# Kernel tuning notes

Hardware: AMD Instinct MI355X
Metric: run time of the kernel (lower is better)

## Reference

```python
import jax, jax.numpy as jnp
import numpy as np

N, F, D, K = 4096, 128, 64, 2  # nodes, in_dim, out_dim, hops


def setup_inputs() -> dict:
    key = jax.random.key(0)
    k_x, k_a, k_e, k_w = jax.random.split(key, 4)
    X = jax.random.normal(k_x, (N, F), jnp.float32)
    # K+1 non-negative dense adjacency/distance matrices (stacked list)
    A = jax.random.uniform(k_a, (K + 1, N, N), jnp.float32)
    # Dense(out_dim, use_bias=False) weights, glorot-like scale
    W_emb = jax.random.normal(k_e, (F, D), jnp.float32) / np.sqrt(F)
    W_hops = jax.random.normal(k_w, (K + 1, F, D), jnp.float32) / np.sqrt(F)
    alpha = jnp.float32(0.1)
    return {"X": X, "A": A, "W_emb": W_emb, "W_hops": W_hops, "alpha": alpha}


def reference(X, A, W_emb, W_hops, alpha):
    # learned embeddings E = Dense(X)  -> [N, D]
    E = X @ W_emb
    # shared low-rank update alpha * E @ E^T  -> [N, N]
    low_rank = alpha * (E @ E.T)
    # per-hop kernel projections Dense_k(X)  -> [K+1, N, D]
    XW = jnp.einsum('nf,kfd->knd', X, W_hops)
    out = jnp.zeros((N, D), X.dtype)
    for k in range(A.shape[0]):  # fixed small K+1 hops
        A_hat = A[k] + low_rank                       # [N, N]
        deg = jnp.sum(A_hat, axis=1)                  # row sums
        d = jnp.power(deg, -0.5)                      # D^{-1/2}
        # D^{-1/2} A_hat D^{-1/2} via broadcast scaling (same math as diag matmuls)
        A_norm = d[:, None] * A_hat * d[None, :]
        out = out + A_norm @ XW[k]
    return jax.nn.relu(out)
```

## Files before the change

kernel.cpp:

```cpp
#include <hip/hip_runtime.h>
#include <math.h>

#define N_ 4096
#define F_ 128
#define D_ 64
#define KH_ 3
#define ZS_ 16
#define KC_ (N_ / ZS_)
#define BM_ 256

#define OFF_E      0
#define OFF_XW     (N_*D_)
#define OFF_SE     (OFF_XW + KH_*N_*D_)
#define OFF_T      (OFF_SE + D_)
#define OFF_RS     (OFF_T + KH_*D_*D_)
#define OFF_DVEC   (OFF_RS + KH_*N_)
#define OFF_YT     (OFF_DVEC + KH_*N_)
#define OFF_AYP    (OFF_YT + KH_*D_*N_/2)
#define OFF_ABF    (OFF_AYP + ZS_*KH_*N_*D_)

typedef __attribute__((ext_vector_type(8))) short bf16x8;
typedef __attribute__((ext_vector_type(4))) float f32x4;

static __device__ __forceinline__ unsigned short f2bf(float f) {
  union { float f; unsigned u; } v; v.f = f;
  unsigned r = (v.u + 0x7fffu + ((v.u >> 16) & 1u)) >> 16;
  return (unsigned short)r;
}

static __device__ __forceinline__ void gload_lds16(const unsigned short* g,
                                                   unsigned short* l) {
  __builtin_amdgcn_global_load_lds(
      (__attribute__((address_space(1))) unsigned int*)g,
      (__attribute__((address_space(3))) unsigned int*)l, 16, 0, 0);
}

__global__ __launch_bounds__(256) void degconv_kernel(
    const float* __restrict__ A, float* __restrict__ ws)
{
  if (blockIdx.x == 0) {
    for (int i = threadIdx.x; i < D_ + KH_ * D_ * D_; i += 256)
      ws[OFF_SE + i] = 0.f;
  }
  int lane = threadIdx.x & 63;
  int wave = threadIdx.x >> 6;
  int row = blockIdx.x * 4 + wave;
  const f32x4* Ar = (const f32x4*)(A + (size_t)row * N_);
  unsigned short* Br = (unsigned short*)(ws + OFF_ABF) + (size_t)row * N_;
  float s = 0.f;
#pragma unroll
  for (int it = 0; it < 8; ++it) {
    f32x4 v0 = __builtin_nontemporal_load(Ar + it * 128 + lane * 2 + 0);
    f32x4 v1 = __builtin_nontemporal_load(Ar + it * 128 + lane * 2 + 1);
    s += (v0[0] + v0[1]) + (v0[2] + v0[3]) + (v1[0] + v1[1]) + (v1[2] + v1[3]);
    union { unsigned short u[8]; uint4 q; } pk;
    pk.u[0] = f2bf(v0[0]); pk.u[1] = f2bf(v0[1]);
    pk.u[2] = f2bf(v0[2]); pk.u[3] = f2bf(v0[3]);
    pk.u[4] = f2bf(v1[0]); pk.u[5] = f2bf(v1[1]);
    pk.u[6] = f2bf(v1[2]); pk.u[7] = f2bf(v1[3]);
    *(uint4*)(Br + (size_t)it * 512 + lane * 8) = pk.q;
  }
#pragma unroll
  for (int off = 32; off > 0; off >>= 1)
    s += __shfl_xor(s, off);
  if (lane == 0) ws[OFF_RS + row] = s;
}

__global__ __launch_bounds__(256) void proj_kernel(
    const float* __restrict__ X, const float* __restrict__ W_emb,
    const float* __restrict__ W_hops, float* __restrict__ ws)
{
  __shared__ __align__(16) float sXT[32][68];
  __shared__ __align__(16) float sW[32][68];
  const int t = threadIdx.x;
  const int m = blockIdx.y;
  const int row0 = blockIdx.x * 64;
  const float* W = (m == 0) ? W_emb : (W_hops + (size_t)(m - 1) * F_ * D_);
  float* out = (m == 0) ? (ws + OFF_E) : (ws + OFF_XW + (size_t)(m - 1) * N_ * D_);
  const int tx = t & 15, ty = t >> 4;
  const int d0 = tx * 4, i0 = ty * 4;
  float acc[4][4] = {};
  for (int fc = 0; fc < F_; fc += 32) {
    {
      int i_l = t >> 3;
      int f_l = (t & 7) * 4;
      for (int r = 0; r < 2; ++r) {
        int i = i_l + r * 32;
        float4 v = *(const float4*)(X + (size_t)(row0 + i) * F_ + fc + f_l);
        sXT[f_l + 0][i] = v.x; sXT[f_l + 1][i] = v.y;
        sXT[f_l + 2][i] = v.z; sXT[f_l + 3][i] = v.w;
      }
      int f2 = t >> 4;
      int d  = (t & 15) * 4;
      for (int r = 0; r < 2; ++r) {
        int f = f2 + r * 16;
        *(float4*)&sW[f][d] = *(const float4*)(W + (size_t)(fc + f) * D_ + d);
      }
    }
    __syncthreads();
#pragma unroll 8
    for (int f = 0; f < 32; ++f) {
      float a[4], b[4];
      *(float4*)a = *(const float4*)&sXT[f][i0];
      *(float4*)b = *(const float4*)&sW[f][d0];
      for (int x = 0; x < 4; ++x)
        for (int y = 0; y < 4; ++y)
          acc[x][y] += a[x] * b[y];
    }
    __syncthreads();
  }
  for (int x = 0; x < 4; ++x)
    *(float4*)(out + (size_t)(row0 + i0 + x) * D_ + d0) = *(float4*)acc[x];
  if (m == 0) {
    float p[4];
    for (int y = 0; y < 4; ++y)
      p[y] = acc[0][y] + acc[1][y] + acc[2][y] + acc[3][y];
    *(float4*)&sXT[ty][d0] = *(float4*)p;
    __syncthreads();
    if (ty < 4) {
      int c = ty * 16 + tx;
      float s = 0.f;
#pragma unroll
      for (int r = 0; r < 16; ++r) s += sXT[r][c];
      atomicAdd(ws + OFF_SE + c, s);
    }
  }
}

__global__ __launch_bounds__(256) void prep_kernel(float* __restrict__ ws,
                                                   const float* __restrict__ alpha_p)
{
  const int k = blockIdx.y;
  const float* XWk = ws + OFF_XW + (size_t)k * N_ * D_;
  const float* E   = ws + OFF_E;
  const float* Sv  = ws + OFF_SE;
  const float* rs  = ws + OFF_RS + (size_t)k * N_;
  const float alpha = *alpha_p;
  int t = threadIdx.x;

  if (blockIdx.x < 64) {
    const int j0 = blockIdx.x * 64;
    unsigned short* Ytk = (unsigned short*)(ws + OFF_YT) + (size_t)k * D_ * N_;
    __shared__ float sS[64];
    __shared__ float d_l[64];
    __shared__ __align__(16) float sEy[64][65];
    __shared__ float sT[64][65];
    if (t < 64) sS[t] = Sv[t];
    {
      int j = t >> 2;
      int c0 = (t & 3) * 16;
      for (int r = 0; r < 4; ++r)
        *(float4*)&sEy[j][c0 + 4 * r] = *(const float4*)(E + (size_t)(j0 + j) * D_ + c0 + 4 * r);
    }
    __syncthreads();
    if (t < 64) {
      float dot = 0.f;
#pragma unroll 16
      for (int c = 0; c < 64; ++c) dot += sEy[t][c] * sS[c];
      float dv = 1.0f / sqrtf(rs[j0 + t] + alpha * dot);
      d_l[t] = dv;
      ws[OFF_DVEC + (size_t)k * N_ + j0 + t] = dv;
    }
    __syncthreads();
    {
      int j = t >> 2;
      int c0 = (t & 3) * 16;
      float dv = d_l[j];
      for (int r = 0; r < 4; ++r) {
        float4 v = *(const float4*)(XWk + (size_t)(j0 + j) * D_ + c0 + 4 * r);
        sT[c0 + 4 * r + 0][j] = v.x * dv;
        sT[c0 + 4 * r + 1][j] = v.y * dv;
        sT[c0 + 4 * r + 2][j] = v.z * dv;
        sT[c0 + 4 * r + 3][j] = v.w * dv;
      }
    }
    __syncthreads();
    {
      int n = t >> 2;
      int jq = (t & 3) * 16;
      __align__(16) unsigned short buf[16];
#pragma unroll
      for (int i = 0; i < 16; ++i) buf[i] = f2bf(sT[n][jq + i]);
      uint4* dst = (uint4*)(Ytk + (size_t)n * N_ + j0 + jq);
      dst[0] = *(uint4*)&buf[0];
      dst[1] = *(uint4*)&buf[8];
    }
  } else {
    __shared__ float sS2[64];
    __shared__ float dl2[128];
    __shared__ __align__(16) float sE[32][68];
    __shared__ __align__(16) float sY[32][68];
    int base0 = (blockIdx.x - 64) * 128;
    if (t < 64) sS2[t] = Sv[t];
    __syncthreads();
    if (t < 128) {
      int jr = base0 + t;
      float dot = 0.f;
#pragma unroll 16
      for (int c = 0; c < 64; ++c) dot += E[(size_t)jr * D_ + c] * sS2[c];
      dl2[t] = 1.0f / sqrtf(rs[jr] + alpha * dot);
    }
    __syncthreads();
    int tx = t & 15, ty = t >> 4;
    int d0 = tx * 4, c0 = ty * 4;
    float acc[4][4] = {};
    for (int sub = 0; sub < 4; ++sub) {
      int base = base0 + sub * 32;
      {
        int i_l = t >> 3;
        int c   = (t & 7) * 4;
        float dv = dl2[sub * 32 + i_l];
        for (int r = 0; r < 2; ++r) {
          int col = c + r * 32;
          *(float4*)&sE[i_l][col] = *(const float4*)(E + (size_t)(base + i_l) * D_ + col);
          float4 y = *(const float4*)(XWk + (size_t)(base + i_l) * D_ + col);
          y.x *= dv; y.y *= dv; y.z *= dv; y.w *= dv;
          *(float4*)&sY[i_l][col] = y;
        }
      }
      __syncthreads();
#pragma unroll 8
      for (int i = 0; i < 32; ++i) {
        float c4[4], y4[4];
        *(float4*)c4 = *(const float4*)&sE[i][c0];
        *(float4*)y4 = *(const float4*)&sY[i][d0];
        for (int a = 0; a < 4; ++a)
          for (int b = 0; b < 4; ++b)
            acc[a][b] += c4[a] * y4[b];
      }
      __syncthreads();
    }
    float* Tk = ws + OFF_T + (size_t)k * D_ * D_;
    for (int a = 0; a < 4; ++a)
      for (int b = 0; b < 4; ++b)
        atomicAdd(&Tk[(c0 + a) * D_ + d0 + b], acc[a][b]);
  }
}

__global__ __launch_bounds__(256, 3) void agemm_kernel(
    const float* __restrict__ ws, float* __restrict__ AYp)
{
  const int k = blockIdx.y;
  const int row0 = blockIdx.x * BM_;
  const int kz0 = blockIdx.z * KC_;
  const unsigned short* Ak = (const unsigned short*)(ws + OFF_ABF) + ((size_t)k << 24);
  const unsigned short* Ytk = (const unsigned short*)(ws + OFF_YT) + (size_t)k * D_ * N_;

  __shared__ __align__(16) unsigned short sA[BM_ * 64];
  __shared__ __align__(16) unsigned short sY[64 * 64];

  const int t = threadIdx.x;
  const int lane = t & 63;
  const int w = t >> 6;
  const int m = lane & 15;
  const int q = lane >> 4;
  const int sr = t >> 3;
  const int sc = t & 7;

  f32x4 acc[4][4];
#pragma unroll
  for (int a = 0; a < 4; ++a)
#pragma unroll
    for (int b = 0; b < 4; ++b) acc[a][b] = (f32x4){0.f, 0.f, 0.f, 0.f};

  for (int kt = 0; kt < KC_; kt += 64) {
#pragma unroll
    for (int j = 0; j < 8; ++j) {
      int r = j * 32 + sr;
      gload_lds16(Ak + (size_t)(row0 + r) * N_ + (kz0 + kt) + ((sc ^ (r & 7)) << 3),
                  &sA[j * 2048 + t * 8]);
    }
#pragma unroll
    for (int j = 0; j < 2; ++j) {
      int r = j * 32 + sr;
      gload_lds16(Ytk + (size_t)r * N_ + (kz0 + kt) + ((sc ^ (r & 7)) << 3),
                  &sY[j * 2048 + t * 8]);
    }
    __syncthreads();
#pragma unroll
    for (int s = 0; s < 2; ++s) {
      bf16x8 av[4], bv[4];
#pragma unroll
      for (int mr = 0; mr < 4; ++mr) {
        int row = w * 64 + mr * 16 + m;
        av[mr] = *(const bf16x8*)&sA[row * 64 + (((s * 4 + q) ^ (row & 7)) << 3)];
      }
#pragma unroll
      for (int nt = 0; nt < 4; ++nt) {
        int n = nt * 16 + m;
        bv[nt] = *(const bf16x8*)&sY[n * 64 + (((s * 4 + q) ^ (n & 7)) << 3)];
      }
#pragma unroll
      for (int mr = 0; mr < 4; ++mr)
#pragma unroll
        for (int nt = 0; nt < 4; ++nt)
          acc[mr][nt] = __builtin_amdgcn_mfma_f32_16x16x32_bf16(av[mr], bv[nt],
                                                                acc[mr][nt], 0, 0, 0);
    }
    __syncthreads();
  }
#pragma unroll
  for (int mr = 0; mr < 4; ++mr) {
    float* outp = AYp + (((size_t)blockIdx.z * KH_ + k) * N_ + row0 + w * 64 + mr * 16) * D_;
#pragma unroll
    for (int nt = 0; nt < 4; ++nt)
#pragma unroll
      for (int r = 0; r < 4; ++r)
        outp[(size_t)(q * 4 + r) * D_ + nt * 16 + m] = acc[mr][nt][r];
  }
}

__global__ __launch_bounds__(256) void epilogue_kernel(
    const float* __restrict__ ws, const float* __restrict__ alpha_p,
    float* __restrict__ out)
{
  int g = blockIdx.x * 256 + threadIdx.x;
  int i = g >> 6, d = g & 63;
  const float* E    = ws + OFF_E;
  const float* T    = ws + OFF_T;
  const float* dvec = ws + OFF_DVEC;
  const float* AYp  = ws + OFF_AYP;
  float alpha = *alpha_p;
  float s = 0.f;
  for (int k = 0; k < KH_; ++k) {
    float ay = 0.f;
#pragma unroll
    for (int jc = 0; jc < ZS_; ++jc)
      ay += AYp[(((size_t)jc * KH_ + k) * N_ + i) * D_ + d];
    float lr = 0.f;
    const float* Tk = T + k * D_ * D_;
#pragma unroll 16
    for (int c = 0; c < D_; ++c)
      lr += E[(size_t)i * D_ + c] * Tk[c * D_ + d];
    s += dvec[k * N_ + i] * (ay + alpha * lr);
  }
  out[g] = fmaxf(s, 0.f);
}

extern "C" void kernel_launch(void* const* d_in, const int* in_sizes, int n_in,
                              void* d_out, int out_size, void* d_ws, size_t ws_size,
                              hipStream_t stream) {
  const float* X      = (const float*)d_in[0];
  const float* A      = (const float*)d_in[1];
  const float* W_emb  = (const float*)d_in[2];
  const float* W_hops = (const float*)d_in[3];
  const float* alpha_p= (const float*)d_in[4];
  float* out = (float*)d_out;
  float* ws  = (float*)d_ws;

  degconv_kernel<<<dim3(KH_ * N_ / 4), 256, 0, stream>>>(A, ws);
  proj_kernel<<<dim3(N_ / 64, 4), 256, 0, stream>>>(X, W_emb, W_hops, ws);
  prep_kernel<<<dim3(96, KH_), 256, 0, stream>>>(ws, alpha_p);
  agemm_kernel<<<dim3(N_ / BM_, KH_, ZS_), 256, 0, stream>>>(ws, ws + OFF_AYP);
  epilogue_kernel<<<dim3(N_ * D_ / 256), 256, 0, stream>>>(ws, alpha_p, out);
}
```

Before: 351.0 us.

## Drop bf16 copy of A, convert in GEMM loads, atomically reduce split-K

The degree kernel no longer writes a bf16 copy of A; the split-K GEMM now reads fp32 A directly through registers, converts it to bf16 and stores it into swizzled LDS. Split-K partial outputs are accumulated with atomicAdd into a single AY buffer instead of a large per-slice buffer that the epilogue had to sum. The degree and projection kernels are merged into one launch, and the embedding column sums use per-block partials instead of atomics. This removes the intermediate bf16 write and re-read and the partial-buffer traffic. In exchange the GEMM reads twice as many bytes for A and loses the direct global-to-LDS async loads, and it adds atomic contention on the output.

```diff
diff --git a/kernel.cpp b/kernel.cpp
--- a/kernel.cpp
+++ b/kernel.cpp
@@ -11,13 +11,12 @@
 
 #define OFF_E      0
 #define OFF_XW     (N_*D_)
-#define OFF_SE     (OFF_XW + KH_*N_*D_)
-#define OFF_T      (OFF_SE + D_)
+#define OFF_SEP    (OFF_XW + KH_*N_*D_)
+#define OFF_T      (OFF_SEP + 64*64)
 #define OFF_RS     (OFF_T + KH_*D_*D_)
 #define OFF_DVEC   (OFF_RS + KH_*N_)
 #define OFF_YT     (OFF_DVEC + KH_*N_)
-#define OFF_AYP    (OFF_YT + KH_*D_*N_/2)
-#define OFF_ABF    (OFF_AYP + ZS_*KH_*N_*D_)
+#define OFF_AY     (OFF_YT + KH_*D_*N_/2)
 
 typedef __attribute__((ext_vector_type(8))) short bf16x8;
 typedef __attribute__((ext_vector_type(4))) float f32x4;
@@ -26,6 +25,13 @@
   union { float f; unsigned u; } v; v.f = f;
   unsigned r = (v.u + 0x7fffu + ((v.u >> 16) & 1u)) >> 16;
   return (unsigned short)r;
+}
+
+static __device__ __forceinline__ uint4 pack8(float4 a, float4 b) {
+  union { unsigned short u[8]; uint4 q; } pk;
+  pk.u[0] = f2bf(a.x); pk.u[1] = f2bf(a.y); pk.u[2] = f2bf(a.z); pk.u[3] = f2bf(a.w);
+  pk.u[4] = f2bf(b.x); pk.u[5] = f2bf(b.y); pk.u[6] = f2bf(b.z); pk.u[7] = f2bf(b.w);
+  return pk.q;
 }
 
 static __device__ __forceinline__ void gload_lds16(const unsigned short* g,
@@ -35,46 +41,37 @@
       (__attribute__((address_space(3))) unsigned int*)l, 16, 0, 0);
 }
 
-__global__ __launch_bounds__(256) void degconv_kernel(
-    const float* __restrict__ A, float* __restrict__ ws)
+__global__ __launch_bounds__(256) void front_kernel(
+    const float* __restrict__ A, const float* __restrict__ X,
+    const float* __restrict__ W_emb, const float* __restrict__ W_hops,
+    float* __restrict__ ws)
 {
-  if (blockIdx.x == 0) {
-    for (int i = threadIdx.x; i < D_ + KH_ * D_ * D_; i += 256)
-      ws[OFF_SE + i] = 0.f;
-  }
-  int lane = threadIdx.x & 63;
-  int wave = threadIdx.x >> 6;
-  int row = blockIdx.x * 4 + wave;
-  const f32x4* Ar = (const f32x4*)(A + (size_t)row * N_);
-  unsigned short* Br = (unsigned short*)(ws + OFF_ABF) + (size_t)row * N_;
-  float s = 0.f;
-#pragma unroll
-  for (int it = 0; it < 8; ++it) {
-    f32x4 v0 = __builtin_nontemporal_load(Ar + it * 128 + lane * 2 + 0);
-    f32x4 v1 = __builtin_nontemporal_load(Ar + it * 128 + lane * 2 + 1);
-    s += (v0[0] + v0[1]) + (v0[2] + v0[3]) + (v1[0] + v1[1]) + (v1[2] + v1[3]);
-    union { unsigned short u[8]; uint4 q; } pk;
-    pk.u[0] = f2bf(v0[0]); pk.u[1] = f2bf(v0[1]);
-    pk.u[2] = f2bf(v0[2]); pk.u[3] = f2bf(v0[3]);
-    pk.u[4] = f2bf(v1[0]); pk.u[5] = f2bf(v1[1]);
-    pk.u[6] = f2bf(v1[2]); pk.u[7] = f2bf(v1[3]);
-    *(uint4*)(Br + (size_t)it * 512 + lane * 8) = pk.q;
-  }
-#pragma unroll
-  for (int off = 32; off > 0; off >>= 1)
-    s += __shfl_xor(s, off);
-  if (lane == 0) ws[OFF_RS + row] = s;
-}
-
-__global__ __launch_bounds__(256) void proj_kernel(
-    const float* __restrict__ X, const float* __restrict__ W_emb,
-    const float* __restrict__ W_hops, float* __restrict__ ws)
-{
+  const int t = threadIdx.x;
+  if (blockIdx.x >= 256) {
+    const int db = blockIdx.x - 256;
+    ws[OFF_AY + db * 256 + t] = 0.f;
+    int lane = t & 63;
+    int wave = t >> 6;
+    int row = db * 4 + wave;
+    const f32x4* Ar = (const f32x4*)(A + (size_t)row * N_);
+    float s = 0.f;
+#pragma unroll
+    for (int it = 0; it < 8; ++it) {
+      f32x4 v0 = Ar[it * 128 + lane * 2 + 0];
+      f32x4 v1 = Ar[it * 128 + lane * 2 + 1];
+      s += (v0[0] + v0[1]) + (v0[2] + v0[3]) + (v1[0] + v1[1]) + (v1[2] + v1[3]);
+    }
+#pragma unroll
+    for (int off = 32; off > 0; off >>= 1)
+      s += __shfl_xor(s, off);
+    if (lane == 0) ws[OFF_RS + row] = s;
+    return;
+  }
   __shared__ __align__(16) float sXT[32][68];
   __shared__ __align__(16) float sW[32][68];
-  const int t = threadIdx.x;
-  const int m = blockIdx.y;
-  const int row0 = blockIdx.x * 64;
+  const int m = blockIdx.x >> 6;
+  const int rb = blockIdx.x & 63;
+  const int row0 = rb * 64;
   const float* W = (m == 0) ? W_emb : (W_hops + (size_t)(m - 1) * F_ * D_);
   float* out = (m == 0) ? (ws + OFF_E) : (ws + OFF_XW + (size_t)(m - 1) * N_ * D_);
   const int tx = t & 15, ty = t >> 4;
@@ -122,8 +119,10 @@
       float s = 0.f;
 #pragma unroll
       for (int r = 0; r < 16; ++r) s += sXT[r][c];
-      atomicAdd(ws + OFF_SE + c, s);
-    }
+      ws[OFF_SEP + rb * 64 + c] = s;
+    }
+    if (rb == 0)
+      for (int i = t; i < KH_ * D_ * D_; i += 256) ws[OFF_T + i] = 0.f;
   }
 }
 
@@ -133,7 +132,6 @@
   const int k = blockIdx.y;
   const float* XWk = ws + OFF_XW + (size_t)k * N_ * D_;
   const float* E   = ws + OFF_E;
-  const float* Sv  = ws + OFF_SE;
   const float* rs  = ws + OFF_RS + (size_t)k * N_;
   const float alpha = *alpha_p;
   int t = threadIdx.x;
@@ -142,24 +140,37 @@
     const int j0 = blockIdx.x * 64;
     unsigned short* Ytk = (unsigned short*)(ws + OFF_YT) + (size_t)k * D_ * N_;
     __shared__ float sS[64];
+    __shared__ float sSp[4][64];
     __shared__ float d_l[64];
     __shared__ __align__(16) float sEy[64][65];
     __shared__ float sT[64][65];
-    if (t < 64) sS[t] = Sv[t];
-    {
-      int j = t >> 2;
-      int c0 = (t & 3) * 16;
+    {
+      int wv = t >> 6, ln = t & 63;
+      float sp = 0.f;
+#pragma unroll
+      for (int r = 0; r < 16; ++r) sp += ws[OFF_SEP + (wv * 16 + r) * 64 + ln];
+      sSp[wv][ln] = sp;
+    }
+    {
+      int j = t >> 2, c0 = (t & 3) * 16;
       for (int r = 0; r < 4; ++r)
         *(float4*)&sEy[j][c0 + 4 * r] = *(const float4*)(E + (size_t)(j0 + j) * D_ + c0 + 4 * r);
     }
     __syncthreads();
-    if (t < 64) {
+    if (t < 64) sS[t] = sSp[0][t] + sSp[1][t] + sSp[2][t] + sSp[3][t];
+    __syncthreads();
+    {
+      int j = t >> 2, c0 = (t & 3) * 16;
       float dot = 0.f;
-#pragma unroll 16
-      for (int c = 0; c < 64; ++c) dot += sEy[t][c] * sS[c];
-      float dv = 1.0f / sqrtf(rs[j0 + t] + alpha * dot);
-      d_l[t] = dv;
-      ws[OFF_DVEC + (size_t)k * N_ + j0 + t] = dv;
+#pragma unroll
+      for (int c = 0; c < 16; ++c) dot += sEy[j][c0 + c] * sS[c0 + c];
+      dot += __shfl_xor(dot, 1);
+      dot += __shfl_xor(dot, 2);
+      if ((t & 3) == 0) {
+        float dv = 1.0f / sqrtf(rs[j0 + j] + alpha * dot);
+        d_l[j] = dv;
+        ws[OFF_DVEC + (size_t)k * N_ + j0 + j] = dv;
+      }
     }
     __syncthreads();
     {
@@ -187,18 +198,29 @@
     }
   } else {
     __shared__ float sS2[64];
+    __shared__ float sSp2[4][64];
     __shared__ float dl2[128];
     __shared__ __align__(16) float sE[32][68];
     __shared__ __align__(16) float sY[32][68];
     int base0 = (blockIdx.x - 64) * 128;
-    if (t < 64) sS2[t] = Sv[t];
-    __syncthreads();
-    if (t < 128) {
-      int jr = base0 + t;
+    {
+      int wv = t >> 6, ln = t & 63;
+      float sp = 0.f;
+#pragma unroll
+      for (int r = 0; r < 16; ++r) sp += ws[OFF_SEP + (wv * 16 + r) * 64 + ln];
+      sSp2[wv][ln] = sp;
+    }
+    __syncthreads();
+    if (t < 64) sS2[t] = sSp2[0][t] + sSp2[1][t] + sSp2[2][t] + sSp2[3][t];
+    __syncthreads();
+    {
+      int jr2 = t >> 1, h = t & 1;
       float dot = 0.f;
-#pragma unroll 16
-      for (int c = 0; c < 64; ++c) dot += E[(size_t)jr * D_ + c] * sS2[c];
-      dl2[t] = 1.0f / sqrtf(rs[jr] + alpha * dot);
+#pragma unroll
+      for (int c = 0; c < 32; ++c)
+        dot += E[(size_t)(base0 + jr2) * D_ + h * 32 + c] * sS2[h * 32 + c];
+      dot += __shfl_xor(dot, 1);
+      if (h == 0) dl2[jr2] = 1.0f / sqrtf(rs[base0 + jr2] + alpha * dot);
     }
     __syncthreads();
     int tx = t & 15, ty = t >> 4;
@@ -238,12 +260,13 @@
 }
 
 __global__ __launch_bounds__(256, 3) void agemm_kernel(
-    const float* __restrict__ ws, float* __restrict__ AYp)
+    const float* __restrict__ A, const float* __restrict__ ws,
+    float* __restrict__ AY)
 {
   const int k = blockIdx.y;
   const int row0 = blockIdx.x * BM_;
   const int kz0 = blockIdx.z * KC_;
-  const unsigned short* Ak = (const unsigned short*)(ws + OFF_ABF) + ((size_t)k << 24);
+  const float* Ak = A + ((size_t)k << 24);
   const unsigned short* Ytk = (const unsigned short*)(ws + OFF_YT) + (size_t)k * D_ * N_;
 
   __shared__ __align__(16) unsigned short sA[BM_ * 64];
@@ -256,6 +279,8 @@
   const int q = lane >> 4;
   const int sr = t >> 3;
   const int sc = t & 7;
+  const int ar = t >> 2;
+  const int ac = t & 3;
 
   f32x4 acc[4][4];
 #pragma unroll
@@ -264,18 +289,24 @@
     for (int b = 0; b < 4; ++b) acc[a][b] = (f32x4){0.f, 0.f, 0.f, 0.f};
 
   for (int kt = 0; kt < KC_; kt += 64) {
-#pragma unroll
-    for (int j = 0; j < 8; ++j) {
-      int r = j * 32 + sr;
-      gload_lds16(Ak + (size_t)(row0 + r) * N_ + (kz0 + kt) + ((sc ^ (r & 7)) << 3),
-                  &sA[j * 2048 + t * 8]);
-    }
 #pragma unroll
     for (int j = 0; j < 2; ++j) {
       int r = j * 32 + sr;
       gload_lds16(Ytk + (size_t)r * N_ + (kz0 + kt) + ((sc ^ (r & 7)) << 3),
                   &sY[j * 2048 + t * 8]);
     }
+#pragma unroll
+    for (int p = 0; p < 4; ++p) {
+      int r = p * 64 + ar;
+      const float* g = Ak + (size_t)(row0 + r) * N_ + (kz0 + kt) + ac * 16;
+      float4 v0 = *(const float4*)(g + 0);
+      float4 v1 = *(const float4*)(g + 4);
+      float4 v2 = *(const float4*)(g + 8);
+      float4 v3 = *(const float4*)(g + 12);
+      int ch0 = 2 * ac, ch1 = ch0 + 1;
+      *(uint4*)&sA[r * 64 + ((ch0 ^ (r & 7)) << 3)] = pack8(v0, v1);
+      *(uint4*)&sA[r * 64 + ((ch1 ^ (r & 7)) << 3)] = pack8(v2, v3);
+    }
     __syncthreads();
 #pragma unroll
     for (int s = 0; s < 2; ++s) {
@@ -301,12 +332,12 @@
   }
 #pragma unroll
   for (int mr = 0; mr < 4; ++mr) {
-    float* outp = AYp + (((size_t)blockIdx.z * KH_ + k) * N_ + row0 + w * 64 + mr * 16) * D_;
+    float* outp = AY + ((size_t)k * N_ + row0 + w * 64 + mr * 16) * D_;
 #pragma unroll
     for (int nt = 0; nt < 4; ++nt)
 #pragma unroll
       for (int r = 0; r < 4; ++r)
-        outp[(size_t)(q * 4 + r) * D_ + nt * 16 + m] = acc[mr][nt][r];
+        atomicAdd(&outp[(size_t)(q * 4 + r) * D_ + nt * 16 + m], acc[mr][nt][r]);
   }
 }
 
@@ -316,23 +347,18 @@
 {
   int g = blockIdx.x * 256 + threadIdx.x;
   int i = g >> 6, d = g & 63;
-  const float* E    = ws + OFF_E;
-  const float* T    = ws + OFF_T;
-  const float* dvec = ws + OFF_DVEC;
-  const float* AYp  = ws + OFF_AYP;
+  const float* E = ws + OFF_E;
   float alpha = *alpha_p;
   float s = 0.f;
+#pragma unroll
   for (int k = 0; k < KH_; ++k) {
-    float ay = 0.f;
-#pragma unroll
-    for (int jc = 0; jc < ZS_; ++jc)
-      ay += AYp[(((size_t)jc * KH_ + k) * N_ + i) * D_ + d];
+    float ay = ws[OFF_AY + ((size_t)k * N_ + i) * D_ + d];
     float lr = 0.f;
-    const float* Tk = T + k * D_ * D_;
+    const float* Tk = ws + OFF_T + k * D_ * D_;
 #pragma unroll 16
     for (int c = 0; c < D_; ++c)
       lr += E[(size_t)i * D_ + c] * Tk[c * D_ + d];
-    s += dvec[k * N_ + i] * (ay + alpha * lr);
+    s += ws[OFF_DVEC + k * N_ + i] * (ay + alpha * lr);
   }
   out[g] = fmaxf(s, 0.f);
 }
@@ -348,9 +374,8 @@
   float* out = (float*)d_out;
   float* ws  = (float*)d_ws;
 
-  degconv_kernel<<<dim3(KH_ * N_ / 4), 256, 0, stream>>>(A, ws);
-  proj_kernel<<<dim3(N_ / 64, 4), 256, 0, stream>>>(X, W_emb, W_hops, ws);
+  front_kernel<<<dim3(256 + KH_ * N_ / 4), 256, 0, stream>>>(A, X, W_emb, W_hops, ws);
   prep_kernel<<<dim3(96, KH_), 256, 0, stream>>>(ws, alpha_p);
-  agemm_kernel<<<dim3(N_ / BM_, KH_, ZS_), 256, 0, stream>>>(ws, ws + OFF_AYP);
+  agemm_kernel<<<dim3(N_ / BM_, KH_, ZS_), 256, 0, stream>>>(A, ws, ws + OFF_AY);
   epilogue_kernel<<<dim3(N_ * D_ / 256), 256, 0, stream>>>(ws, alpha_p, out);
 }
```

After: 376.8 us. +7.3%, slower.
